# Kernel optimization log

Measured on AMD Instinct MI355X. Metric: run time of the kernel, lower is better.

Reference implementation:

```python
import jax, jax.numpy as jnp
import numpy as np
import math

DIM = 4096
N_HEADS = 32
N_KV_HEADS = 8
HEAD_DIM = DIM // N_HEADS
N_REP = N_HEADS // N_KV_HEADS
ROPE_BASE = 10000.0


def apply_rotary_emb(x):
    # x: [b, s, h, d] -> rotate pairs (LLaMA-style complex rotation)
    b, s, h, d = x.shape
    inv_freq = 1.0 / (ROPE_BASE ** (jnp.arange(0, d, 2, dtype=jnp.float32) / d))  # [d/2]
    pos = jnp.arange(s, dtype=jnp.float32)
    ang = pos[:, None] * inv_freq[None, :]          # [s, d/2]
    cos = jnp.cos(ang)[None, :, None, :]            # [1, s, 1, d/2]
    sin = jnp.sin(ang)[None, :, None, :]
    xr = x.reshape(b, s, h, d // 2, 2)
    x0, x1 = xr[..., 0], xr[..., 1]
    out = jnp.stack([x0 * cos - x1 * sin, x0 * sin + x1 * cos], axis=-1)
    return out.reshape(b, s, h, d)


def setup_inputs() -> dict:
    key = jax.random.key(0)
    ks = jax.random.split(key, 5)
    sc = 1.0 / math.sqrt(DIM)
    return {
        "x": jax.random.normal(ks[0], (2, 2048, DIM), dtype=jnp.float32),
        "Wq": jax.random.normal(ks[1], (DIM, N_HEADS * HEAD_DIM), dtype=jnp.float32) * sc,
        "Wk": jax.random.normal(ks[2], (DIM, N_KV_HEADS * HEAD_DIM), dtype=jnp.float32) * sc,
        "Wv": jax.random.normal(ks[3], (DIM, N_KV_HEADS * HEAD_DIM), dtype=jnp.float32) * sc,
        "Wo": jax.random.normal(ks[4], (N_HEADS * HEAD_DIM, DIM), dtype=jnp.float32) * sc,
    }


def reference(x, Wq, Wk, Wv, Wo):
    b, s, _ = x.shape
    xq = (x @ Wq).reshape(b, s, N_HEADS, HEAD_DIM)
    xk = (x @ Wk).reshape(b, s, N_KV_HEADS, HEAD_DIM)
    xv = (x @ Wv).reshape(b, s, N_KV_HEADS, HEAD_DIM)
    xq = apply_rotary_emb(xq)
    xk = apply_rotary_emb(xk)
    # GQA: repeat kv heads
    xk = jnp.repeat(xk, N_REP, axis=2)  # [b, s, H, d]
    xv = jnp.repeat(xv, N_REP, axis=2)
    scores = jnp.einsum('bqhd,bkhd->bhqk', xq, xk) / math.sqrt(HEAD_DIM)
    causal = jnp.tril(jnp.ones((s, s), dtype=bool))
    scores = jnp.where(causal[None, None], scores, -jnp.inf)
    probs = jax.nn.softmax(scores.astype(jnp.float32), axis=-1).astype(xq.dtype)
    out = jnp.einsum('bhqk,bkhd->bqhd', probs, xv).reshape(b, s, N_HEADS * HEAD_DIM)
    return out @ Wo  # dropout is identity in eval
```

## Files before the change

### kernel.cpp

```cpp
#include <hip/hip_runtime.h>
#include <hip/hip_bf16.h>

typedef __attribute__((ext_vector_type(8))) short short8;
typedef __attribute__((ext_vector_type(4))) float f32x4;

typedef const void __attribute__((address_space(1)))* gptr_t;
typedef void __attribute__((address_space(3)))* sptr_t;

static __device__ __forceinline__ void gload_lds16(const void* g, void* l) {
  __builtin_amdgcn_global_load_lds((gptr_t)g, (sptr_t)l, 16, 0, 0);
}

static __device__ __forceinline__ unsigned short f2bf(float f) {
  unsigned int u = __float_as_uint(f);
  unsigned int r = (u + 0x7fffu + ((u >> 16) & 1u)) >> 16;
  return (unsigned short)r;
}
static __device__ __forceinline__ float bf2f(unsigned short b) {
  return __uint_as_float(((unsigned int)b) << 16);
}
static __device__ __forceinline__ unsigned int cvt_pk_bf16(float lo, float hi) {
  unsigned int r;
  asm("v_cvt_pk_bf16_f32 %0, %1, %2" : "=v"(r) : "v"(lo), "v"(hi));
  return r;
}

__global__ void cvt_f32_to_bf16(const float* __restrict__ in,
                                unsigned short* __restrict__ out, int n) {
  int idx = blockIdx.x * blockDim.x + threadIdx.x;
  int stride = gridDim.x * blockDim.x;
  for (int i = idx * 4; i < n; i += stride * 4) {
    const float4 v = *reinterpret_cast<const float4*>(in + i);
    unsigned long long packed =
        (unsigned long long)f2bf(v.x) | ((unsigned long long)f2bf(v.y) << 16) |
        ((unsigned long long)f2bf(v.z) << 32) | ((unsigned long long)f2bf(v.w) << 48);
    *reinterpret_cast<unsigned long long*>(out + i) = packed;
  }
}

__global__ void cvt_transpose_bf16(const float* __restrict__ in,
                                   unsigned short* __restrict__ out, int K, int N) {
  __shared__ unsigned short tile[32][33];
  int kt = blockIdx.y * 32, nt = blockIdx.x * 32;
  int tx = threadIdx.x & 31;
  int ty = threadIdx.x >> 5;
  #pragma unroll
  for (int i = 0; i < 32; i += 8)
    tile[ty + i][tx] = f2bf(in[(size_t)(kt + ty + i) * N + nt + tx]);
  __syncthreads();
  #pragma unroll
  for (int i = 0; i < 32; i += 8)
    out[(size_t)(nt + ty + i) * K + kt + tx] = tile[tx][ty + i];
}

__global__ void transpose_v(const unsigned short* __restrict__ Vp,
                            unsigned short* __restrict__ VT, int vstride) {
  __shared__ unsigned short tile[32][33];
  int st = blockIdx.x * 32;
  int dt = blockIdx.y * 32;
  int bh = blockIdx.z;
  int b = bh >> 3, h = bh & 7;
  int tx = threadIdx.x & 31, ty = threadIdx.x >> 5;
  #pragma unroll
  for (int i = 0; i < 32; i += 8)
    tile[ty + i][tx] = Vp[(size_t)(b * 2048 + st + ty + i) * vstride + h * 128 + dt + tx];
  __syncthreads();
  #pragma unroll
  for (int i = 0; i < 32; i += 8)
    VT[(size_t)((b * 8 + h) * 128 + dt + ty + i) * 2048 + st + tx] = tile[tx][ty + i];
}

__global__ void rope_kernel(unsigned short* __restrict__ buf, int rows, int nheads,
                            int rowstride, float oscale) {
  int total = rows * nheads * 64;
  int idx = blockIdx.x * blockDim.x + threadIdx.x;
  if (idx >= total) return;
  int j = idx & 63;
  int hh = (idx >> 6) % nheads;
  int r = idx / (64 * nheads);
  int pos = r & 2047;
  float inv = expf(-(float)j * 0.14391157f);
  float ang = (float)pos * inv;
  float s, c;
  sincosf(ang, &s, &c);
  unsigned int* p =
      reinterpret_cast<unsigned int*>(buf + (size_t)r * rowstride + hh * 128 + 2 * j);
  unsigned int pv = *p;
  float x0 = bf2f((unsigned short)(pv & 0xffffu));
  float x1 = bf2f((unsigned short)(pv >> 16));
  float o0 = (x0 * c - x1 * s) * oscale;
  float o1 = (x0 * s + x1 * c) * oscale;
  *p = (unsigned int)f2bf(o0) | ((unsigned int)f2bf(o1) << 16);
}

static __device__ __forceinline__ void store_out(unsigned short* C, size_t idx, float v) {
  C[idx] = f2bf(v);
}
static __device__ __forceinline__ void store_out(float* C, size_t idx, float v) {
  C[idx] = v;
}

template <typename OutT>
__global__ __launch_bounds__(512) void gemm_8ph(const unsigned short* __restrict__ A,
                                                const unsigned short* __restrict__ BT,
                                                OutT* __restrict__ C, int M, int N,
                                                int K) {
  __shared__ __align__(16) unsigned short S[2][4][8192];
  const int tid = threadIdx.x;
  const int w = tid >> 6, lane = tid & 63;
  const int fr = lane & 15, fg = lane >> 4;
  const int wr = w >> 2, wc = w & 3;

  const int nbx = N >> 8;
  const int bid = blockIdx.x;
  const int cpx = gridDim.x >> 3;
  const int lid = (bid & 7) * cpx + (bid >> 3);
  const int brow = lid / nbx, bcol = lid % nbx;

  const int sr8 = lane >> 3;
  const int sc8 = lane & 7;
  const int sgc = sc8 ^ sr8;
  const unsigned short* gA = A + (size_t)(brow * 256) * K;
  const unsigned short* gB = BT + (size_t)(bcol * 256) * K;
  const int NT = K >> 6;

  f32x4 acc[8][4] = {};

  auto stageHT = [&](int t, int ht) {
    if (t >= NT) t -= NT;
    const unsigned short* src = (ht < 2) ? gA : gB;
    const int half = ht & 1;
    unsigned short* dst = &S[t & 1][ht][0];
    #pragma unroll
    for (int l = 0; l < 2; l++) {
      const int rl = w * 16 + l * 8;
      gload_lds16(src + (size_t)(half * 128 + rl + sr8) * K + t * 64 + sgc * 8,
                  dst + rl * 64);
    }
  };

  stageHT(0, 0);
  stageHT(0, 1);
  stageHT(0, 2);
  stageHT(0, 3);
  stageHT(1, 2);
  stageHT(1, 3);
  asm volatile("s_waitcnt vmcnt(4)" ::: "memory");
  __builtin_amdgcn_s_barrier();

  const int rdswz = fr & 7;
  for (int t = 0; t < NT; t++) {
    const unsigned short* Sa = &S[t & 1][wr][0];
    const unsigned short* Sb = &S[t & 1][2 + (wc >> 1)][0];
    short8 bfr[4][2];
    #pragma unroll
    for (int q = 0; q < 4; q++) {
      short8 a[2][2];
      #pragma unroll
      for (int i = 0; i < 2; i++)
        #pragma unroll
        for (int ks = 0; ks < 2; ks++) {
          const int row = (2 * q + i) * 16 + fr;
          a[i][ks] = *reinterpret_cast<const short8*>(
              &Sa[row * 64 + ((ks * 4 + fg) ^ rdswz) * 8]);
        }
      if (q == 0) {
        #pragma unroll
        for (int n = 0; n < 4; n++)
          #pragma unroll
          for (int ks = 0; ks < 2; ks++) {
            const int row = (wc & 1) * 64 + n * 16 + fr;
            bfr[n][ks] = *reinterpret_cast<const short8*>(
                &Sb[row * 64 + ((ks * 4 + fg) ^ rdswz) * 8]);
          }
      }
      if (q < 2)
        stageHT(t + 1, q);
      else
        stageHT(t + 2, q);
      __builtin_amdgcn_s_barrier();
      asm volatile("s_waitcnt lgkmcnt(0)" ::: "memory");
      __builtin_amdgcn_sched_barrier(0);
      __builtin_amdgcn_s_setprio(1);
      #pragma unroll
      for (int i = 0; i < 2; i++)
        #pragma unroll
        for (int n = 0; n < 4; n++) {
          acc[2 * q + i][n] =
              __builtin_amdgcn_mfma_f32_16x16x32_bf16(a[i][0], bfr[n][0],
                                                      acc[2 * q + i][n], 0, 0, 0);
          acc[2 * q + i][n] =
              __builtin_amdgcn_mfma_f32_16x16x32_bf16(a[i][1], bfr[n][1],
                                                      acc[2 * q + i][n], 0, 0, 0);
        }
      __builtin_amdgcn_s_setprio(0);
      if (q == 3) asm volatile("s_waitcnt vmcnt(4)" ::: "memory");
      __builtin_amdgcn_s_barrier();
    }
  }
  asm volatile("s_waitcnt vmcnt(0)" ::: "memory");

  #pragma unroll
  for (int i = 0; i < 8; i++)
    #pragma unroll
    for (int n = 0; n < 4; n++)
      #pragma unroll
      for (int r = 0; r < 4; r++) {
        int row = brow * 256 + wr * 128 + i * 16 + fg * 4 + r;
        int col = bcol * 256 + wc * 64 + n * 16 + fr;
        store_out(C, (size_t)row * N + col, acc[i][n][r]);
      }
}

template <int AM, typename OutT>
__global__ __launch_bounds__(512) void gemm_bt256(const unsigned short* __restrict__ A,
                                                  const unsigned short* __restrict__ BT,
                                                  OutT* __restrict__ C, int M, int N,
                                                  int K) {
  constexpr int H = AM / 4;
  __shared__ __align__(16) unsigned short S[4][(AM + 16) * 512];
  const int tid = threadIdx.x;
  const int w = tid >> 6, lane = tid & 63;
  const int fr = lane & 15, fg = lane >> 4;
  const int wr = w >> 2, wc = w & 3;

  const int nbx = N >> 8;
  const int bid = blockIdx.x;
  const int cpx = gridDim.x >> 3;
  const int lid = (bid & 7) * cpx + (bid >> 3);
  const int brow = lid / nbx, bcol = lid % nbx;

  const int srl = lane >> 2;
  const int scc = (lane & 3) ^ (((lane >> 5) & 1) << 1);
  const unsigned short* gA = A + (size_t)(brow * (AM * 16)) * K;
  const unsigned short* gB = BT + (size_t)(bcol * 256) * K;

  f32x4 acc[2 * H][4] = {};
  const int rdoff = fr * 32 + ((fg ^ (((fr >> 3) & 1) << 1)) * 8);

  const int NT = K >> 5;

  for (int s = 0; s < 3; s++) {
    const int kb = s * 32;
    #pragma unroll
    for (int u = 0; u < AM / 8; u++) {
      int sb = (AM / 8) * w + u;
      gload_lds16(gA + (size_t)(sb * 16 + srl) * K + kb + scc * 8, &S[s][sb * 512]);
    }
    #pragma unroll
    for (int u = 0; u < 2; u++) {
      int sb = 2 * w + u;
      gload_lds16(gB + (size_t)(sb * 16 + srl) * K + kb + scc * 8,
                  &S[s][AM * 512 + sb * 512]);
    }
  }
  asm volatile("s_waitcnt vmcnt(6)" ::: "memory");
  __builtin_amdgcn_s_barrier();

  for (int s = 0; s < NT; s++) {
    const unsigned short* Sa = &S[s & 3][0];
    const unsigned short* Sb = &S[s & 3][AM * 512];
    const int bufn = (s + 3) & 3;
    int kn = s + 3;
    if (kn >= NT) kn -= NT;
    const int kbn = kn * 32;

    short8 b[4], a0[H], a1[H];
    #pragma unroll
    for (int j = 0; j < 4; j++)
      b[j] = *reinterpret_cast<const short8*>(&Sb[(wc * 4 + j) * 512 + rdoff]);
    #pragma unroll
    for (int i = 0; i < H; i++)
      a0[i] = *reinterpret_cast<const short8*>(&Sa[(wr * 2 * H + i) * 512 + rdoff]);
    #pragma unroll
    for (int i = 0; i < H; i++)
      a1[i] = *reinterpret_cast<const short8*>(&Sa[(wr * 2 * H + H + i) * 512 + rdoff]);
    #pragma unroll
    for (int u = 0; u < AM / 8; u++) {
      int sb = (AM / 8) * w + u;
      gload_lds16(gA + (size_t)(sb * 16 + srl) * K + kbn + scc * 8, &S[bufn][sb * 512]);
    }
    #pragma unroll
    for (int u = 0; u < 2; u++) {
      int sb = 2 * w + u;
      gload_lds16(gB + (size_t)(sb * 16 + srl) * K + kbn + scc * 8,
                  &S[bufn][AM * 512 + sb * 512]);
    }
    asm volatile("s_waitcnt lgkmcnt(2)" ::: "memory");
    __builtin_amdgcn_sched_barrier(0);
    __builtin_amdgcn_s_setprio(1);
    #pragma unroll
    for (int i = 0; i < H; i++)
      #pragma unroll
      for (int j = 0; j < 4; j++)
        acc[i][j] = __builtin_amdgcn_mfma_f32_16x16x32_bf16(a0[i], b[j], acc[i][j], 0, 0, 0);
    __builtin_amdgcn_s_setprio(0);
    __builtin_amdgcn_sched_barrier(0);
    asm volatile("s_waitcnt lgkmcnt(0)" ::: "memory");
    __builtin_amdgcn_sched_barrier(0);
    __builtin_amdgcn_s_setprio(1);
    #pragma unroll
    for (int i = 0; i < H; i++)
      #pragma unroll
      for (int j = 0; j < 4; j++)
        acc[H + i][j] =
            __builtin_amdgcn_mfma_f32_16x16x32_bf16(a1[i], b[j], acc[H + i][j], 0, 0, 0);
    __builtin_amdgcn_s_setprio(0);
    asm volatile("s_waitcnt vmcnt(6)" ::: "memory");
    __builtin_amdgcn_s_barrier();
  }

  #pragma unroll
  for (int i = 0; i < 2 * H; i++)
    #pragma unroll
    for (int j = 0; j < 4; j++)
      #pragma unroll
      for (int r = 0; r < 4; r++) {
        int row = brow * (AM * 16) + wr * (AM * 8) + i * 16 + fg * 4 + r;
        int col = bcol * 256 + wc * 64 + j * 16 + fr;
        store_out(C, (size_t)row * N + col, acc[i][j][r]);
      }
}

__global__ __launch_bounds__(256, 2) void flash_attn(const unsigned short* __restrict__ Q,
                                                     const unsigned short* __restrict__ KV,
                                                     const unsigned short* __restrict__ VT,
                                                     unsigned short* __restrict__ O) {
  __shared__ __align__(16) unsigned short K_lds[2][64][128];
  __shared__ __align__(16) unsigned short V_lds[2][128][64];
  __shared__ __align__(16) unsigned short P_lds[4][16][68];

  const int wave = threadIdx.x >> 6, lane = threadIdx.x & 63;
  const int fr = lane & 15, fg = lane >> 4;

  const int bid = blockIdx.x;
  const int lid = (bid & 7) * 64 + (bid >> 3);
  const int pr = lid & 7;
  const int h = (lid >> 3) & 31;
  const int b = lid >> 8;
  const int kvh = h >> 2;

  const unsigned short* Qb = Q + (size_t)(b * 2048) * 4096 + h * 128;
  const unsigned short* Kb = KV + (size_t)(b * 2048) * 2048 + kvh * 128;
  const unsigned short* Vb = VT + (size_t)((b * 8 + kvh) * 128) * 2048;

  const int l4 = lane >> 4, c16 = lane & 15;
  const int l3 = lane >> 3, c8 = lane & 7;

  auto stage = [&](int kb, int bf) {
    #pragma unroll
    for (int c = 0; c < 4; c++) {
      int rl = wave * 16 + c * 4 + l4;
      int ch = c16 ^ (rl & 7);
      gload_lds16(Kb + (size_t)(kb + rl) * 2048 + ch * 8, &K_lds[bf][wave * 16 + c * 4][0]);
    }
    #pragma unroll
    for (int c = 0; c < 4; c++) {
      int rl = wave * 32 + c * 8 + l3;
      int ch = c8 ^ (rl & 7);
      gload_lds16(Vb + (size_t)rl * 2048 + kb + ch * 8, &V_lds[bf][wave * 32 + c * 8][0]);
    }
  };

  for (int seg = 0; seg < 2; seg++) {
    const int blk = seg ? pr : 15 - pr;
    const int qw = blk * 128 + wave * 32;

    short8 qf[2][4];
    #pragma unroll
    for (int m = 0; m < 2; m++)
      #pragma unroll
      for (int dk = 0; dk < 4; dk++)
        qf[m][dk] = *reinterpret_cast<const short8*>(
            &Qb[(size_t)(qw + m * 16 + fr) * 4096 + dk * 32 + fg * 8]);

    float mrow[2] = {-INFINITY, -INFINITY};
    float lrow[2] = {0.f, 0.f};
    f32x4 oacc[2][8] = {};

    const int nt = 2 * blk + 2;
    stage(0, 0);

    for (int t = 0; t < nt; t++) {
      const int kb = t * 64;
      if (t + 1 < nt) {
        stage((t + 1) * 64, (t + 1) & 1);
        asm volatile("s_waitcnt vmcnt(8)" ::: "memory");
      } else {
        asm volatile("s_waitcnt vmcnt(0)" ::: "memory");
      }
      __builtin_amdgcn_s_barrier();

      if (kb <= qw + 31) {
        const unsigned short* Kl = &K_lds[t & 1][0][0];
        const unsigned short* Vl = &V_lds[t & 1][0][0];

        f32x4 s[2][4] = {};
        #pragma unroll
        for (int kc = 0; kc < 4; kc++) {
          short8 kf[4];
          #pragma unroll
          for (int dk = 0; dk < 4; dk++)
            kf[dk] = *reinterpret_cast<const short8*>(
                &Kl[(kc * 16 + fr) * 128 + (((dk * 4 + fg) ^ (fr & 7)) << 3)]);
          #pragma unroll
          for (int dk = 0; dk < 4; dk++) {
            s[0][kc] =
                __builtin_amdgcn_mfma_f32_16x16x32_bf16(kf[dk], qf[0][dk], s[0][kc], 0, 0, 0);
            s[1][kc] =
                __builtin_amdgcn_mfma_f32_16x16x32_bf16(kf[dk], qf[1][dk], s[1][kc], 0, 0, 0);
          }
        }
        if (kb + 63 > qw) {
          #pragma unroll
          for (int m = 0; m < 2; m++) {
            const int qi = qw + m * 16 + fr;
            #pragma unroll
            for (int kc = 0; kc < 4; kc++)
              #pragma unroll
              for (int r = 0; r < 4; r++)
                if (kb + kc * 16 + fg * 4 + r > qi) s[m][kc][r] = -INFINITY;
          }
        }

        short8 pf[2][2];
        #pragma unroll
        for (int m = 0; m < 2; m++) {
          float mx = -INFINITY;
          #pragma unroll
          for (int kc = 0; kc < 4; kc++)
            #pragma unroll
            for (int r = 0; r < 4; r++) mx = fmaxf(mx, s[m][kc][r]);
          mx = fmaxf(mx, __shfl_xor(mx, 16));
          mx = fmaxf(mx, __shfl_xor(mx, 32));
          const bool need = !__all(mx - mrow[m] <= 8.0f);
          float mnew = need ? fmaxf(mrow[m], mx) : mrow[m];
          if (need) {
            float alpha = exp2f(mrow[m] - mnew);
            lrow[m] *= alpha;
            float alw[4];
            #pragma unroll
            for (int r = 0; r < 4; r++) alw[r] = __shfl(alpha, fg * 4 + r);
            #pragma unroll
            for (int dt = 0; dt < 8; dt++)
              #pragma unroll
              for (int r = 0; r < 4; r++) oacc[m][dt][r] *= alw[r];
          }
          float p_[16];
          float rs = 0.f;
          #pragma unroll
          for (int kc = 0; kc < 4; kc++)
            #pragma unroll
            for (int r = 0; r < 4; r++) {
              float pv = exp2f(s[m][kc][r] - mnew);
              p_[kc * 4 + r] = pv;
              rs += pv;
            }
          rs += __shfl_xor(rs, 16);
          rs += __shfl_xor(rs, 32);
          lrow[m] += rs;
          mrow[m] = mnew;
          #pragma unroll
          for (int kc = 0; kc < 4; kc++) {
            unsigned int lo = cvt_pk_bf16(p_[kc * 4 + 0], p_[kc * 4 + 1]);
            unsigned int hi = cvt_pk_bf16(p_[kc * 4 + 2], p_[kc * 4 + 3]);
            unsigned int* dst =
                reinterpret_cast<unsigned int*>(&P_lds[wave][fr][kc * 16 + fg * 4]);
            dst[0] = lo;
            dst[1] = hi;
          }
          pf[m][0] = *reinterpret_cast<const short8*>(&P_lds[wave][fr][fg * 8]);
          pf[m][1] = *reinterpret_cast<const short8*>(&P_lds[wave][fr][32 + fg * 8]);
        }

        #pragma unroll
        for (int c = 0; c < 2; c++)
          #pragma unroll
          for (int dt = 0; dt < 8; dt++) {
            short8 vf = *reinterpret_cast<const short8*>(
                &Vl[(dt * 16 + fr) * 64 + (((c * 4 + fg) ^ (fr & 7)) << 3)]);
            oacc[0][dt] =
                __builtin_amdgcn_mfma_f32_16x16x32_bf16(pf[0][c], vf, oacc[0][dt], 0, 0, 0);
            oacc[1][dt] =
                __builtin_amdgcn_mfma_f32_16x16x32_bf16(pf[1][c], vf, oacc[1][dt], 0, 0, 0);
          }
      }
      __builtin_amdgcn_s_barrier();
    }

    #pragma unroll
    for (int m = 0; m < 2; m++) {
      float linv[4];
      #pragma unroll
      for (int r = 0; r < 4; r++) linv[r] = 1.0f / __shfl(lrow[m], fg * 4 + r);
      #pragma unroll
      for (int dt = 0; dt < 8; dt++)
        #pragma unroll
        for (int r = 0; r < 4; r++) {
          int row = qw + m * 16 + fg * 4 + r;
          float v = oacc[m][dt][r] * linv[r];
          O[(size_t)(b * 2048 + row) * 4096 + h * 128 + dt * 16 + fr] = f2bf(v);
        }
    }
  }
}

extern "C" void kernel_launch(void* const* d_in, const int* in_sizes, int n_in,
                              void* d_out, int out_size, void* d_ws, size_t ws_size,
                              hipStream_t stream) {
  const float* x = (const float*)d_in[0];
  const float* Wq = (const float*)d_in[1];
  const float* Wk = (const float*)d_in[2];
  const float* Wv = (const float*)d_in[3];
  const float* Wo = (const float*)d_in[4];
  float* out = (float*)d_out;

  char* ws = (char*)d_ws;
  unsigned short* xb   = (unsigned short*)(ws + 0);
  unsigned short* WqT  = (unsigned short*)(ws + 33554432);
  unsigned short* WkvT = (unsigned short*)(ws + 67108864);
  unsigned short* WoT  = (unsigned short*)(ws + 83886080);
  unsigned short* Qb   = (unsigned short*)(ws + 117440512);
  unsigned short* KVb  = (unsigned short*)(ws + 150994944);
  unsigned short* VT   = (unsigned short*)(ws + 167772160);
  unsigned short* Ob   = (unsigned short*)(ws + 176160768);

  cvt_f32_to_bf16<<<2048, 256, 0, stream>>>(x, xb, 4096 * 4096);
  cvt_transpose_bf16<<<dim3(128, 128), 256, 0, stream>>>(Wq, WqT, 4096, 4096);
  cvt_transpose_bf16<<<dim3(32, 128), 256, 0, stream>>>(Wk, WkvT, 4096, 1024);
  cvt_transpose_bf16<<<dim3(32, 128), 256, 0, stream>>>(Wv, WkvT + (size_t)1024 * 4096,
                                                        4096, 1024);
  cvt_transpose_bf16<<<dim3(128, 128), 256, 0, stream>>>(Wo, WoT, 4096, 4096);

  gemm_8ph<unsigned short><<<256, 512, 0, stream>>>(xb, WqT, Qb, 4096, 4096, 4096);
  gemm_bt256<8, unsigned short><<<256, 512, 0, stream>>>(xb, WkvT, KVb, 4096, 2048, 4096);

  rope_kernel<<<(4096 * 32 * 64 + 255) / 256, 256, 0, stream>>>(Qb, 4096, 32, 4096,
                                                                0.12751780f);
  rope_kernel<<<(4096 * 8 * 64 + 255) / 256, 256, 0, stream>>>(KVb, 4096, 8, 2048, 1.0f);

  transpose_v<<<dim3(64, 4, 16), 256, 0, stream>>>(KVb + 1024, VT, 2048);

  flash_attn<<<512, 256, 0, stream>>>(Qb, KVb, VT, Ob);

  gemm_8ph<float><<<256, 512, 0, stream>>>(Ob, WoT, out, 4096, 4096, 4096);
}
```

Before: 510.9 us.

## Split flash attention into 8 waves with 16 query rows each

The attention kernel goes from 4 waves handling 32 query rows each to 8 waves handling 16 rows each, with 512 threads per block. Staging of the K and V tiles is split across the 8 waves, so each wave issues half as many loads and the vmcnt wait changes to match. Per-wave register state (Q fragments, accumulators, softmax stats) is halved to allow more waves in flight and better latency hiding. In exchange, each K and V fragment read from LDS now feeds only one MFMA instead of two, so LDS traffic per FLOP doubles, and the block-wide barriers now synchronise twice as many waves.

```diff
diff --git a/kernel.cpp b/kernel.cpp
--- a/kernel.cpp
+++ b/kernel.cpp
@@ -322,13 +322,13 @@
       }
 }
 
-__global__ __launch_bounds__(256, 2) void flash_attn(const unsigned short* __restrict__ Q,
+__global__ __launch_bounds__(512, 4) void flash_attn(const unsigned short* __restrict__ Q,
                                                      const unsigned short* __restrict__ KV,
                                                      const unsigned short* __restrict__ VT,
                                                      unsigned short* __restrict__ O) {
   __shared__ __align__(16) unsigned short K_lds[2][64][128];
   __shared__ __align__(16) unsigned short V_lds[2][128][64];
-  __shared__ __align__(16) unsigned short P_lds[4][16][68];
+  __shared__ __align__(16) unsigned short P_lds[8][16][36];
 
   const int wave = threadIdx.x >> 6, lane = threadIdx.x & 63;
   const int fr = lane & 15, fg = lane >> 4;
@@ -349,34 +349,32 @@
 
   auto stage = [&](int kb, int bf) {
     #pragma unroll
-    for (int c = 0; c < 4; c++) {
-      int rl = wave * 16 + c * 4 + l4;
+    for (int c = 0; c < 2; c++) {
+      int rl = wave * 8 + c * 4 + l4;
       int ch = c16 ^ (rl & 7);
-      gload_lds16(Kb + (size_t)(kb + rl) * 2048 + ch * 8, &K_lds[bf][wave * 16 + c * 4][0]);
-    }
-    #pragma unroll
-    for (int c = 0; c < 4; c++) {
-      int rl = wave * 32 + c * 8 + l3;
+      gload_lds16(Kb + (size_t)(kb + rl) * 2048 + ch * 8, &K_lds[bf][wave * 8 + c * 4][0]);
+    }
+    #pragma unroll
+    for (int c = 0; c < 2; c++) {
+      int rl = wave * 16 + c * 8 + l3;
       int ch = c8 ^ (rl & 7);
-      gload_lds16(Vb + (size_t)rl * 2048 + kb + ch * 8, &V_lds[bf][wave * 32 + c * 8][0]);
+      gload_lds16(Vb + (size_t)rl * 2048 + kb + ch * 8, &V_lds[bf][wave * 16 + c * 8][0]);
     }
   };
 
   for (int seg = 0; seg < 2; seg++) {
     const int blk = seg ? pr : 15 - pr;
-    const int qw = blk * 128 + wave * 32;
-
-    short8 qf[2][4];
-    #pragma unroll
-    for (int m = 0; m < 2; m++)
-      #pragma unroll
-      for (int dk = 0; dk < 4; dk++)
-        qf[m][dk] = *reinterpret_cast<const short8*>(
-            &Qb[(size_t)(qw + m * 16 + fr) * 4096 + dk * 32 + fg * 8]);
-
-    float mrow[2] = {-INFINITY, -INFINITY};
-    float lrow[2] = {0.f, 0.f};
-    f32x4 oacc[2][8] = {};
+    const int qw = blk * 128 + wave * 16;
+
+    short8 qf[4];
+    #pragma unroll
+    for (int dk = 0; dk < 4; dk++)
+      qf[dk] = *reinterpret_cast<const short8*>(
+          &Qb[(size_t)(qw + fr) * 4096 + dk * 32 + fg * 8]);
+
+    float mrow = -INFINITY;
+    float lrow = 0.f;
+    f32x4 oacc[8] = {};
 
     const int nt = 2 * blk + 2;
     stage(0, 0);
@@ -385,17 +383,17 @@
       const int kb = t * 64;
       if (t + 1 < nt) {
         stage((t + 1) * 64, (t + 1) & 1);
-        asm volatile("s_waitcnt vmcnt(8)" ::: "memory");
+        asm volatile("s_waitcnt vmcnt(4)" ::: "memory");
       } else {
         asm volatile("s_waitcnt vmcnt(0)" ::: "memory");
       }
       __builtin_amdgcn_s_barrier();
 
-      if (kb <= qw + 31) {
+      if (kb <= qw + 15) {
         const unsigned short* Kl = &K_lds[t & 1][0][0];
         const unsigned short* Vl = &V_lds[t & 1][0][0];
 
-        f32x4 s[2][4] = {};
+        f32x4 s[4] = {};
         #pragma unroll
         for (int kc = 0; kc < 4; kc++) {
           short8 kf[4];
@@ -404,73 +402,67 @@
             kf[dk] = *reinterpret_cast<const short8*>(
                 &Kl[(kc * 16 + fr) * 128 + (((dk * 4 + fg) ^ (fr & 7)) << 3)]);
           #pragma unroll
-          for (int dk = 0; dk < 4; dk++) {
-            s[0][kc] =
-                __builtin_amdgcn_mfma_f32_16x16x32_bf16(kf[dk], qf[0][dk], s[0][kc], 0, 0, 0);
-            s[1][kc] =
-                __builtin_amdgcn_mfma_f32_16x16x32_bf16(kf[dk], qf[1][dk], s[1][kc], 0, 0, 0);
-          }
+          for (int dk = 0; dk < 4; dk++)
+            s[kc] = __builtin_amdgcn_mfma_f32_16x16x32_bf16(kf[dk], qf[dk], s[kc], 0, 0, 0);
         }
         if (kb + 63 > qw) {
-          #pragma unroll
-          for (int m = 0; m < 2; m++) {
-            const int qi = qw + m * 16 + fr;
-            #pragma unroll
-            for (int kc = 0; kc < 4; kc++)
-              #pragma unroll
-              for (int r = 0; r < 4; r++)
-                if (kb + kc * 16 + fg * 4 + r > qi) s[m][kc][r] = -INFINITY;
-          }
-        }
-
-        short8 pf[2][2];
-        #pragma unroll
-        for (int m = 0; m < 2; m++) {
-          float mx = -INFINITY;
+          const int qi = qw + fr;
           #pragma unroll
           for (int kc = 0; kc < 4; kc++)
             #pragma unroll
-            for (int r = 0; r < 4; r++) mx = fmaxf(mx, s[m][kc][r]);
-          mx = fmaxf(mx, __shfl_xor(mx, 16));
-          mx = fmaxf(mx, __shfl_xor(mx, 32));
-          const bool need = !__all(mx - mrow[m] <= 8.0f);
-          float mnew = need ? fmaxf(mrow[m], mx) : mrow[m];
-          if (need) {
-            float alpha = exp2f(mrow[m] - mnew);
-            lrow[m] *= alpha;
-            float alw[4];
+            for (int r = 0; r < 4; r++)
+              if (kb + kc * 16 + fg * 4 + r > qi) s[kc][r] = -INFINITY;
+        }
+
+        float mx = -INFINITY;
+        #pragma unroll
+        for (int kc = 0; kc < 4; kc++)
+          #pragma unroll
+          for (int r = 0; r < 4; r++) mx = fmaxf(mx, s[kc][r]);
+        mx = fmaxf(mx, __shfl_xor(mx, 16));
+        mx = fmaxf(mx, __shfl_xor(mx, 32));
+        const bool need = !__all(mx - mrow <= 8.0f);
+        float mnew = need ? fmaxf(mrow, mx) : mrow;
+        if (need) {
+          float alpha = exp2f(mrow - mnew);
+          lrow *= alpha;
+          float alw[4];
+          #pragma unroll
+          for (int r = 0; r < 4; r++) alw[r] = __shfl(alpha, fg * 4 + r);
+          #pragma unroll
+          for (int dt = 0; dt < 8; dt++)
             #pragma unroll
-            for (int r = 0; r < 4; r++) alw[r] = __shfl(alpha, fg * 4 + r);
-            #pragma unroll
-            for (int dt = 0; dt < 8; dt++)
-              #pragma unroll
-              for (int r = 0; r < 4; r++) oacc[m][dt][r] *= alw[r];
+            for (int r = 0; r < 4; r++) oacc[dt][r] *= alw[r];
+        }
+        float p_[16];
+        float rs = 0.f;
+        #pragma unroll
+        for (int kc = 0; kc < 4; kc++)
+          #pragma unroll
+          for (int r = 0; r < 4; r++) {
+            float pv = exp2f(s[kc][r] - mnew);
+            p_[kc * 4 + r] = pv;
+            rs += pv;
           }
-          float p_[16];
-          float rs = 0.f;
-          #pragma unroll
-          for (int kc = 0; kc < 4; kc++)
-            #pragma unroll
-            for (int r = 0; r < 4; r++) {
-              float pv = exp2f(s[m][kc][r] - mnew);
-              p_[kc * 4 + r] = pv;
-              rs += pv;
-            }
-          rs += __shfl_xor(rs, 16);
-          rs += __shfl_xor(rs, 32);
-          lrow[m] += rs;
-          mrow[m] = mnew;
-          #pragma unroll
-          for (int kc = 0; kc < 4; kc++) {
-            unsigned int lo = cvt_pk_bf16(p_[kc * 4 + 0], p_[kc * 4 + 1]);
-            unsigned int hi = cvt_pk_bf16(p_[kc * 4 + 2], p_[kc * 4 + 3]);
+        rs += __shfl_xor(rs, 16);
+        rs += __shfl_xor(rs, 32);
+        lrow += rs;
+        mrow = mnew;
+
+        short8 pf[2];
+        #pragma unroll
+        for (int half = 0; half < 2; half++) {
+          #pragma unroll
+          for (int kc = 0; kc < 2; kc++) {
+            int kk = half * 2 + kc;
+            unsigned int lo = cvt_pk_bf16(p_[kk * 4 + 0], p_[kk * 4 + 1]);
+            unsigned int hi = cvt_pk_bf16(p_[kk * 4 + 2], p_[kk * 4 + 3]);
             unsigned int* dst =
                 reinterpret_cast<unsigned int*>(&P_lds[wave][fr][kc * 16 + fg * 4]);
             dst[0] = lo;
             dst[1] = hi;
           }
-          pf[m][0] = *reinterpret_cast<const short8*>(&P_lds[wave][fr][fg * 8]);
-          pf[m][1] = *reinterpret_cast<const short8*>(&P_lds[wave][fr][32 + fg * 8]);
+          pf[half] = *reinterpret_cast<const short8*>(&P_lds[wave][fr][fg * 8]);
         }
 
         #pragma unroll
@@ -479,29 +471,23 @@
           for (int dt = 0; dt < 8; dt++) {
             short8 vf = *reinterpret_cast<const short8*>(
                 &Vl[(dt * 16 + fr) * 64 + (((c * 4 + fg) ^ (fr & 7)) << 3)]);
-            oacc[0][dt] =
-                __builtin_amdgcn_mfma_f32_16x16x32_bf16(pf[0][c], vf, oacc[0][dt], 0, 0, 0);
-            oacc[1][dt] =
-                __builtin_amdgcn_mfma_f32_16x16x32_bf16(pf[1][c], vf, oacc[1][dt], 0, 0, 0);
+            oacc[dt] = __builtin_amdgcn_mfma_f32_16x16x32_bf16(pf[c], vf, oacc[dt], 0, 0, 0);
           }
       }
       __builtin_amdgcn_s_barrier();
     }
 
-    #pragma unroll
-    for (int m = 0; m < 2; m++) {
-      float linv[4];
-      #pragma unroll
-      for (int r = 0; r < 4; r++) linv[r] = 1.0f / __shfl(lrow[m], fg * 4 + r);
-      #pragma unroll
-      for (int dt = 0; dt < 8; dt++)
-        #pragma unroll
-        for (int r = 0; r < 4; r++) {
-          int row = qw + m * 16 + fg * 4 + r;
-          float v = oacc[m][dt][r] * linv[r];
-          O[(size_t)(b * 2048 + row) * 4096 + h * 128 + dt * 16 + fr] = f2bf(v);
-        }
-    }
+    float linv[4];
+    #pragma unroll
+    for (int r = 0; r < 4; r++) linv[r] = 1.0f / __shfl(lrow, fg * 4 + r);
+    #pragma unroll
+    for (int dt = 0; dt < 8; dt++)
+      #pragma unroll
+      for (int r = 0; r < 4; r++) {
+        int row = qw + fg * 4 + r;
+        float v = oacc[dt][r] * linv[r];
+        O[(size_t)(b * 2048 + row) * 4096 + h * 128 + dt * 16 + fr] = f2bf(v);
+      }
   }
 }
 
@@ -541,7 +527,7 @@
 
   transpose_v<<<dim3(64, 4, 16), 256, 0, stream>>>(KVb + 1024, VT, 2048);
 
-  flash_attn<<<512, 256, 0, stream>>>(Qb, KVb, VT, Ob);
+  flash_attn<<<512, 512, 0, stream>>>(Qb, KVb, VT, Ob);
 
   gemm_8ph<float><<<256, 512, 0, stream>>>(Ob, WoT, out, 4096, 4096, 4096);
 }
```

New measurement: 513.2 us. No clear change (+0.4%).
